# Performance work log

Measured on AMD Instinct MI355X. Metric: run time of the kernel, lower is better.

## Reference

```python
import jax, jax.numpy as jnp
import numpy as np

H_IN, W_IN = 192, 192
H_OUT, W_OUT = 96, 96
B = 1024


def setup_inputs() -> dict:
    key = jax.random.key(0)
    k1, k2 = jax.random.split(key)
    x = jax.random.normal(k1, (B, 1, H_IN, W_IN), dtype=jnp.float32)
    # z_where = [s, tx, ty]; uniform [0,1) keeps s nonnegative, translations in-range
    z_where = jax.random.uniform(k2, (B, 3), dtype=jnp.float32)
    return {"x": x, "z_where": z_where}


def z_where_to_matrix(z_where):
    # [[s, 0, tx], [0, s, ty]]  (inverse=False path)
    s, tx, ty = z_where[:, 0], z_where[:, 1], z_where[:, 2]
    zero = jnp.zeros_like(s)
    row0 = jnp.stack([s, zero, tx], axis=-1)
    row1 = jnp.stack([zero, s, ty], axis=-1)
    return jnp.stack([row0, row1], axis=1)  # (B, 2, 3)


def affine_grid(theta, Ho, Wo):
    # PyTorch F.affine_grid with align_corners=False (default)
    xs = (2.0 * (jnp.arange(Wo, dtype=jnp.float32) + 0.5) / Wo) - 1.0
    ys = (2.0 * (jnp.arange(Ho, dtype=jnp.float32) + 0.5) / Ho) - 1.0
    gy, gx = jnp.meshgrid(ys, xs, indexing="ij")  # (Ho, Wo)
    base = jnp.stack([gx, gy, jnp.ones_like(gx)], axis=-1)  # (Ho, Wo, 3)
    # grid[b,h,w,i] = sum_k theta[b,i,k] * base[h,w,k]
    return jnp.einsum("hwk,bik->bhwi", base, theta)  # (B, Ho, Wo, 2)


def grid_sample_bilinear_zeros(x, grid):
    # PyTorch F.grid_sample: mode='bilinear', padding_mode='zeros', align_corners=False
    Bn, C, H, W = x.shape
    gx, gy = grid[..., 0], grid[..., 1]
    ix = ((gx + 1.0) * W - 1.0) * 0.5
    iy = ((gy + 1.0) * H - 1.0) * 0.5
    ix0 = jnp.floor(ix)
    iy0 = jnp.floor(iy)
    wx1 = ix - ix0
    wy1 = iy - iy0
    wx0 = 1.0 - wx1
    wy0 = 1.0 - wy1
    ix0i = ix0.astype(jnp.int32)
    iy0i = iy0.astype(jnp.int32)
    ix1i = ix0i + 1
    iy1i = iy0i + 1

    imgs = x[:, 0]  # (B, H, W) single channel

    def sample_one(img, yi, xi):
        valid = (yi >= 0) & (yi < H) & (xi >= 0) & (xi < W)
        yc = jnp.clip(yi, 0, H - 1)
        xc = jnp.clip(xi, 0, W - 1)
        return img[yc, xc] * valid.astype(img.dtype)

    gather = jax.vmap(sample_one)  # over batch
    v00 = gather(imgs, iy0i, ix0i)
    v01 = gather(imgs, iy0i, ix1i)
    v10 = gather(imgs, iy1i, ix0i)
    v11 = gather(imgs, iy1i, ix1i)
    out = (wy0 * wx0 * v00 + wy0 * wx1 * v01 +
           wy1 * wx0 * v10 + wy1 * wx1 * v11)
    return out[:, None, :, :]  # (B, 1, Ho, Wo)


def reference(x, z_where):
    theta = z_where_to_matrix(z_where)
    grid = affine_grid(theta, H_OUT, W_OUT)
    return grid_sample_bilinear_zeros(x, grid)
```

## Files before the change

kernel.cpp:

```cpp
#include <hip/hip_runtime.h>


#define H_IN   192
#define W_IN   192
#define H_OUT  96
#define W_OUT  96
#define PX_PER_IMG   (H_OUT * W_OUT)
#define BLOCK        256
#define BLOCKS_PER_IMG (PX_PER_IMG / BLOCK)

__global__ __launch_bounds__(BLOCK) void st_bilinear_kernel(
    const float* __restrict__ x,
    const float* __restrict__ zw,
    float* __restrict__ out)
{
    const int b = blockIdx.x / BLOCKS_PER_IMG;
    const int p = (blockIdx.x % BLOCKS_PER_IMG) * BLOCK + threadIdx.x;
    const int oy = p / W_OUT;
    const int ox = p - oy * W_OUT;

    const float s  = zw[b * 3 + 0];
    const float tx = zw[b * 3 + 1];
    const float ty = zw[b * 3 + 2];

    const float xs = 2.0f * ((float)ox + 0.5f) / (float)W_OUT - 1.0f;
    const float ys = 2.0f * ((float)oy + 0.5f) / (float)H_OUT - 1.0f;
    const float gx = s * xs + tx;
    const float gy = s * ys + ty;

    const float ix = ((gx + 1.0f) * (float)W_IN - 1.0f) * 0.5f;
    const float iy = ((gy + 1.0f) * (float)H_IN - 1.0f) * 0.5f;

    const float ix0f = floorf(ix);
    const float iy0f = floorf(iy);
    const float wx1 = ix - ix0f;
    const float wy1 = iy - iy0f;
    const float wx0 = 1.0f - wx1;
    const float wy0 = 1.0f - wy1;

    const int ix0 = (int)ix0f;
    const int iy0 = (int)iy0f;
    const int ix1 = ix0 + 1;
    const int iy1 = iy0 + 1;

    const float* __restrict__ img = x + (size_t)b * (H_IN * W_IN);

    auto samp = [&](int yi, int xi) -> float {
        const bool valid = (yi >= 0) & (yi < H_IN) & (xi >= 0) & (xi < W_IN);
        const int yc = min(max(yi, 0), H_IN - 1);
        const int xc = min(max(xi, 0), W_IN - 1);
        const float v = img[yc * W_IN + xc];
        return valid ? v : 0.0f;
    };

    const float v00 = samp(iy0, ix0);
    const float v01 = samp(iy0, ix1);
    const float v10 = samp(iy1, ix0);
    const float v11 = samp(iy1, ix1);

    out[(size_t)b * PX_PER_IMG + p] =
        wy0 * wx0 * v00 + wy0 * wx1 * v01 +
        wy1 * wx0 * v10 + wy1 * wx1 * v11;
}

extern "C" void kernel_launch(void* const* d_in, const int* in_sizes, int n_in,
                              void* d_out, int out_size, void* d_ws, size_t ws_size,
                              hipStream_t stream) {
    const float* x  = (const float*)d_in[0];
    const float* zw = (const float*)d_in[1];
    float* out = (float*)d_out;

    const int B = in_sizes[1] / 3;
    const int grid = B * BLOCKS_PER_IMG;
    st_bilinear_kernel<<<grid, BLOCK, 0, stream>>>(x, zw, out);
}
```

Baseline: 216.7 us.

## Process four output rows per thread with hoisted x-coordinates and batched gathers

Each thread now computes one output column for four consecutive rows. The x interpolation index, weights and validity are computed once and reused across those rows. All sixteen gather loads are issued before any blending so more memory requests are in flight, and the coordinate math is folded into fused multiply-adds. The block size becomes 192 on a 2D grid, which gives fewer threads and more work per thread, with some added register use.

```diff
diff --git a/kernel.cpp b/kernel.cpp
--- a/kernel.cpp
+++ b/kernel.cpp
@@ -5,62 +5,83 @@
 #define W_IN   192
 #define H_OUT  96
 #define W_OUT  96
-#define PX_PER_IMG   (H_OUT * W_OUT)
-#define BLOCK        256
-#define BLOCKS_PER_IMG (PX_PER_IMG / BLOCK)
+#define PX_PER_IMG      (H_OUT * W_OUT)
+#define BLOCK           192
+#define ROWS_PER_THREAD 4
+#define ROWS_PER_BLOCK  8
+#define BLOCKS_PER_IMG  (H_OUT / ROWS_PER_BLOCK)
 
-__global__ __launch_bounds__(BLOCK) void st_bilinear_kernel(
+__global__ __launch_bounds__(BLOCK) void st_bilinear_col_kernel(
     const float* __restrict__ x,
     const float* __restrict__ zw,
     float* __restrict__ out)
 {
-    const int b = blockIdx.x / BLOCKS_PER_IMG;
-    const int p = (blockIdx.x % BLOCKS_PER_IMG) * BLOCK + threadIdx.x;
-    const int oy = p / W_OUT;
-    const int ox = p - oy * W_OUT;
+    const int b  = blockIdx.y;
+    const int t  = threadIdx.x;
+    const int ox = t % W_OUT;
+    const int oy0 = blockIdx.x * ROWS_PER_BLOCK + (t / W_OUT) * ROWS_PER_THREAD;
 
     const float s  = zw[b * 3 + 0];
     const float tx = zw[b * 3 + 1];
     const float ty = zw[b * 3 + 2];
 
-    const float xs = 2.0f * ((float)ox + 0.5f) / (float)W_OUT - 1.0f;
-    const float ys = 2.0f * ((float)oy + 0.5f) / (float)H_OUT - 1.0f;
-    const float gx = s * xs + tx;
-    const float gy = s * ys + ty;
+    const float A  = 2.0f * s;
+    const float C0 = fmaf(-95.0f, s, 95.5f);
+    const float Bx = fmaf(96.0f, tx, C0);
+    const float By = fmaf(96.0f, ty, C0);
 
-    const float ix = ((gx + 1.0f) * (float)W_IN - 1.0f) * 0.5f;
-    const float iy = ((gy + 1.0f) * (float)H_IN - 1.0f) * 0.5f;
-
+    const float ix   = fmaf(A, (float)ox, Bx);
     const float ix0f = floorf(ix);
-    const float iy0f = floorf(iy);
-    const float wx1 = ix - ix0f;
-    const float wy1 = iy - iy0f;
-    const float wx0 = 1.0f - wx1;
-    const float wy0 = 1.0f - wy1;
-
-    const int ix0 = (int)ix0f;
-    const int iy0 = (int)iy0f;
-    const int ix1 = ix0 + 1;
-    const int iy1 = iy0 + 1;
+    const float wx1  = ix - ix0f;
+    const float wx0  = 1.0f - wx1;
+    const int   ix0  = (int)ix0f;
+    const int   ix1  = ix0 + 1;
+    const bool  x0v  = (unsigned)ix0 < (unsigned)W_IN;
+    const bool  x1v  = (unsigned)ix1 < (unsigned)W_IN;
+    const int   xc0  = min(max(ix0, 0), W_IN - 1);
+    const int   xc1  = min(max(ix1, 0), W_IN - 1);
 
     const float* __restrict__ img = x + (size_t)b * (H_IN * W_IN);
+    float* __restrict__ op = out + (size_t)b * PX_PER_IMG + oy0 * W_OUT + ox;
 
-    auto samp = [&](int yi, int xi) -> float {
-        const bool valid = (yi >= 0) & (yi < H_IN) & (xi >= 0) & (xi < W_IN);
-        const int yc = min(max(yi, 0), H_IN - 1);
-        const int xc = min(max(xi, 0), W_IN - 1);
-        const float v = img[yc * W_IN + xc];
-        return valid ? v : 0.0f;
-    };
+    float wy0[ROWS_PER_THREAD], wy1[ROWS_PER_THREAD];
+    int   r0[ROWS_PER_THREAD], r1[ROWS_PER_THREAD];
+    bool  y0v[ROWS_PER_THREAD], y1v[ROWS_PER_THREAD];
 
-    const float v00 = samp(iy0, ix0);
-    const float v01 = samp(iy0, ix1);
-    const float v10 = samp(iy1, ix0);
-    const float v11 = samp(iy1, ix1);
+#pragma unroll
+    for (int j = 0; j < ROWS_PER_THREAD; ++j) {
+        const float iy   = fmaf(A, (float)(oy0 + j), By);
+        const float iy0f = floorf(iy);
+        wy1[j] = iy - iy0f;
+        wy0[j] = 1.0f - wy1[j];
+        const int iy0 = (int)iy0f;
+        const int iy1 = iy0 + 1;
+        y0v[j] = (unsigned)iy0 < (unsigned)H_IN;
+        y1v[j] = (unsigned)iy1 < (unsigned)H_IN;
+        r0[j] = min(max(iy0, 0), H_IN - 1) * W_IN;
+        r1[j] = min(max(iy1, 0), H_IN - 1) * W_IN;
+    }
 
-    out[(size_t)b * PX_PER_IMG + p] =
-        wy0 * wx0 * v00 + wy0 * wx1 * v01 +
-        wy1 * wx0 * v10 + wy1 * wx1 * v11;
+    float v00[ROWS_PER_THREAD], v01[ROWS_PER_THREAD];
+    float v10[ROWS_PER_THREAD], v11[ROWS_PER_THREAD];
+#pragma unroll
+    for (int j = 0; j < ROWS_PER_THREAD; ++j) {
+        v00[j] = img[r0[j] + xc0];
+        v01[j] = img[r0[j] + xc1];
+        v10[j] = img[r1[j] + xc0];
+        v11[j] = img[r1[j] + xc1];
+    }
+
+#pragma unroll
+    for (int j = 0; j < ROWS_PER_THREAD; ++j) {
+        const float a00 = (y0v[j] && x0v) ? v00[j] : 0.0f;
+        const float a01 = (y0v[j] && x1v) ? v01[j] : 0.0f;
+        const float a10 = (y1v[j] && x0v) ? v10[j] : 0.0f;
+        const float a11 = (y1v[j] && x1v) ? v11[j] : 0.0f;
+        const float h0 = wx0 * a00 + wx1 * a01;
+        const float h1 = wx0 * a10 + wx1 * a11;
+        op[j * W_OUT] = wy0[j] * h0 + wy1[j] * h1;
+    }
 }
 
 extern "C" void kernel_launch(void* const* d_in, const int* in_sizes, int n_in,
@@ -71,6 +92,6 @@
     float* out = (float*)d_out;
 
     const int B = in_sizes[1] / 3;
-    const int grid = B * BLOCKS_PER_IMG;
-    st_bilinear_kernel<<<grid, BLOCK, 0, stream>>>(x, zw, out);
+    dim3 grid(BLOCKS_PER_IMG, B);
+    st_bilinear_col_kernel<<<grid, BLOCK, 0, stream>>>(x, zw, out);
 }
```

Result: faster. 204.4 us (-5.7%).
